# Optimization experiments

Measured on AMD Instinct MI355X. Metric: run time of the kernel, lower is better.

Reference implementation:

```python
import jax, jax.numpy as jnp
import numpy as np

B = 4          # batch
C_FEAT = 32    # shared feature channels
N_PARTS = 24   # body parts
H = 256        # triplane resolution (W = 3*H, three planes concatenated on width)
N_PTS = 8192   # sampled points per batch element
C = C_FEAT + N_PARTS


def setup_inputs() -> dict:
    key = jax.random.key(0)
    k1, k2 = jax.random.split(key)
    triplane = jax.random.normal(k1, (B, C, H, 3 * H), dtype=jnp.float32)
    # canonical coords in [-1, 1], one row per (point, part)
    triplane_coord_3d = jax.random.uniform(
        k2, (B * N_PTS * N_PARTS, 3), dtype=jnp.float32, minval=-1.0, maxval=1.0)
    index = jnp.arange(B * N_PTS, dtype=jnp.int32).reshape(B, N_PTS)
    return {"triplane": triplane, "triplane_coord_3d": triplane_coord_3d, "index": index}


def _bilinear(planes, uv):
    """planes: (B, 3, C, H, H); uv: (B, P, 3, 2) in [-1,1] (x->width, y->height).
    align_corners=False, border-clamped bilinear sample. Returns (B, P, 3, C)."""
    Hs = planes.shape[-1]
    px = (uv[..., 0] + 1.0) * (Hs * 0.5) - 0.5
    py = (uv[..., 1] + 1.0) * (Hs * 0.5) - 0.5
    x0f = jnp.floor(px)
    y0f = jnp.floor(py)
    wx = px - x0f
    wy = py - y0f
    x0 = jnp.clip(x0f.astype(jnp.int32), 0, Hs - 1)
    x1 = jnp.clip(x0f.astype(jnp.int32) + 1, 0, Hs - 1)
    y0 = jnp.clip(y0f.astype(jnp.int32), 0, Hs - 1)
    y1 = jnp.clip(y0f.astype(jnp.int32) + 1, 0, Hs - 1)
    bi = jnp.arange(planes.shape[0])[:, None, None]   # (B,1,1)
    ki = jnp.arange(3)[None, None, :]                 # (1,1,3)

    def g(yi, xi):
        return planes[bi, ki, :, yi, xi]              # (B, P, 3, C)

    return (g(y0, x0) * ((1 - wx) * (1 - wy))[..., None]
            + g(y0, x1) * (wx * (1 - wy))[..., None]
            + g(y1, x0) * ((1 - wx) * wy)[..., None]
            + g(y1, x1) * (wx * wy)[..., None])


def reference(triplane, triplane_coord_3d, index):
    Bq, n = index.shape
    # split width into the 3 concatenated planes -> (B, 3, C, H, H)
    planes = triplane.reshape(Bq, C, H, 3, H).transpose(0, 3, 1, 2, 4)
    # per-(point, part) coordinate rows
    rows = index[..., None] * N_PARTS + jnp.arange(N_PARTS, dtype=index.dtype)  # (B,n,P)
    xyz = triplane_coord_3d[rows]                                 # (B, n, P, 3)
    # plane uv: xy, xz, yz
    uv = jnp.stack([xyz[..., jnp.array([0, 1])],
                    xyz[..., jnp.array([0, 2])],
                    xyz[..., jnp.array([1, 2])]], axis=-2)        # (B, n, P, 3, 2)
    uv = uv.reshape(Bq, n * N_PARTS, 3, 2)
    samp = _bilinear(planes, uv).sum(axis=2)                      # sum over 3 planes -> (B, nP, C)
    samp = samp.reshape(Bq, n, N_PARTS, C)
    part_feature = samp[..., :C_FEAT].mean(axis=-1)               # (B, n, P)
    # part p's probability logit is channel 32+p sampled at part p's coords
    logits = samp[:, :, jnp.arange(N_PARTS), C_FEAT + jnp.arange(N_PARTS)]
    part_prob = jax.nn.softmax(logits, axis=-1)                   # (B, n, P)
    return (part_prob * part_feature).sum(axis=-1)                # (B, n)
```

## Files before the change

### kernel.cpp

```cpp
#include <hip/hip_runtime.h>

#define HS 256
#define W3 768
#define CCH 56
#define CF 32
#define NP 24
#define NPTS 8192
#define PLANE_SZ (HS * W3)

__global__ void tp_mean_kernel(const float* __restrict__ tri,
                               float* __restrict__ M) {
    int i4 = blockIdx.x * blockDim.x + threadIdx.x;
    int b = i4 / (PLANE_SZ / 4);
    int rem = i4 % (PLANE_SZ / 4);
    const float4* in = (const float4*)tri + (size_t)b * CCH * (PLANE_SZ / 4) + rem;
    float4 acc = {0.f, 0.f, 0.f, 0.f};
#pragma unroll
    for (int c = 0; c < CF; ++c) {
        float4 v = in[(size_t)c * (PLANE_SZ / 4)];
        acc.x += v.x; acc.y += v.y; acc.z += v.z; acc.w += v.w;
    }
    const float s = 1.0f / (float)CF;
    acc.x *= s; acc.y *= s; acc.z *= s; acc.w *= s;
    ((float4*)M)[(size_t)b * (PLANE_SZ / 4) + rem] = acc;
}

__global__ __launch_bounds__(192) void tp_sample_kernel(
    const float* __restrict__ tri, const float* __restrict__ coords,
    const int* __restrict__ index, const float* __restrict__ M,
    float* __restrict__ out) {
    __shared__ float s_feat[8][NP];
    __shared__ float s_log[8][NP];

    const int tid = threadIdx.x;
    const int lp = tid / NP;
    const int part = tid % NP;
    const int point = blockIdx.x * 8 + lp;
    const int b = point >> 13;

    const int idx = index[point];
    const int row = idx * NP + part;
    const float x = coords[row * 3 + 0];
    const float y = coords[row * 3 + 1];
    const float z = coords[row * 3 + 2];

    const float us[3] = {x, x, y};
    const float vs[3] = {y, z, z};

    const float* __restrict__ Mb = M + (size_t)b * PLANE_SZ;
    const float* __restrict__ Tb = tri + (size_t)(b * CCH + CF + part) * PLANE_SZ;

    float feat = 0.f, lg = 0.f;
#pragma unroll
    for (int k = 0; k < 3; ++k) {
        const float px = (us[k] + 1.0f) * (HS * 0.5f) - 0.5f;
        const float py = (vs[k] + 1.0f) * (HS * 0.5f) - 0.5f;
        const float x0f = floorf(px);
        const float y0f = floorf(py);
        const float wx = px - x0f;
        const float wy = py - y0f;
        const int x0 = min(max((int)x0f, 0), HS - 1);
        const int x1 = min(max((int)x0f + 1, 0), HS - 1);
        const int y0 = min(max((int)y0f, 0), HS - 1);
        const int y1 = min(max((int)y0f + 1, 0), HS - 1);
        const float w00 = (1.f - wx) * (1.f - wy);
        const float w01 = wx * (1.f - wy);
        const float w10 = (1.f - wx) * wy;
        const float w11 = wx * wy;
        const int o00 = y0 * W3 + k * HS + x0;
        const int o01 = y0 * W3 + k * HS + x1;
        const int o10 = y1 * W3 + k * HS + x0;
        const int o11 = y1 * W3 + k * HS + x1;
        feat += Mb[o00] * w00 + Mb[o01] * w01 + Mb[o10] * w10 + Mb[o11] * w11;
        lg   += Tb[o00] * w00 + Tb[o01] * w01 + Tb[o10] * w10 + Tb[o11] * w11;
    }

    s_feat[lp][part] = feat;
    s_log[lp][part] = lg;
    __syncthreads();

    if (tid < 8) {
        float mx = -1e30f;
#pragma unroll
        for (int j = 0; j < NP; ++j) mx = fmaxf(mx, s_log[tid][j]);
        float se = 0.f, acc = 0.f;
#pragma unroll
        for (int j = 0; j < NP; ++j) {
            const float e = __expf(s_log[tid][j] - mx);
            se += e;
            acc += e * s_feat[tid][j];
        }
        out[blockIdx.x * 8 + tid] = acc / se;
    }
}

extern "C" void kernel_launch(void* const* d_in, const int* in_sizes, int n_in,
                              void* d_out, int out_size, void* d_ws, size_t ws_size,
                              hipStream_t stream) {
    const float* tri = (const float*)d_in[0];
    const float* coords = (const float*)d_in[1];
    const int* index = (const int*)d_in[2];
    float* out = (float*)d_out;
    float* M = (float*)d_ws;

    tp_mean_kernel<<<(4 * PLANE_SZ / 4) / 256, 256, 0, stream>>>(tri, M);

    tp_sample_kernel<<<4096, 192, 0, stream>>>(tri, coords, index, M, out);
}
```

Before: 308.9 us.

## Regroup sampling by (batch, part) slab with XCD-aware block swizzle, separate softmax kernel

The gather kernel now gives each workgroup a single (batch, part) slab of 256 points. All threads then read the same logit channel plane, which should improve L2 locality on the 768 KB part planes. Block indices are swizzled in groups of 8, apparently so that neighbouring logical chunks of a slab land on the same XCD. Per-part features and logits are written to workspace, and a second kernel does the softmax reduction over parts with strided loads. This adds a kernel launch and about 6 MB of extra workspace traffic.

```diff
diff --git a/kernel.cpp b/kernel.cpp
--- a/kernel.cpp
+++ b/kernel.cpp
@@ -7,6 +7,10 @@
 #define NP 24
 #define NPTS 8192
 #define PLANE_SZ (HS * W3)
+#define NB 4
+#define NSLAB (NB * NP)
+#define CHUNKS (NPTS / 256)
+#define NWG_B1 (NSLAB * CHUNKS)
 
 __global__ void tp_mean_kernel(const float* __restrict__ tri,
                                float* __restrict__ M) {
@@ -25,18 +29,18 @@
     ((float4*)M)[(size_t)b * (PLANE_SZ / 4) + rem] = acc;
 }
 
-__global__ __launch_bounds__(192) void tp_sample_kernel(
+__global__ __launch_bounds__(256) void tp_gather_kernel(
     const float* __restrict__ tri, const float* __restrict__ coords,
     const int* __restrict__ index, const float* __restrict__ M,
-    float* __restrict__ out) {
-    __shared__ float s_feat[8][NP];
-    __shared__ float s_log[8][NP];
-
-    const int tid = threadIdx.x;
-    const int lp = tid / NP;
-    const int part = tid % NP;
-    const int point = blockIdx.x * 8 + lp;
-    const int b = point >> 13;
+    float* __restrict__ Wf, float* __restrict__ Wl) {
+    const int phys = blockIdx.x;
+    const int l = (phys & 7) * (NWG_B1 / 8) + (phys >> 3);
+    const int slab = l >> 5;
+    const int chunk = l & 31;
+    const int b = slab / NP;
+    const int part = slab - b * NP;
+    const int n = chunk * 256 + threadIdx.x;
+    const int point = b * NPTS + n;
 
     const int idx = index[point];
     const int row = idx * NP + part;
@@ -75,23 +79,34 @@
         lg   += Tb[o00] * w00 + Tb[o01] * w01 + Tb[o10] * w10 + Tb[o11] * w11;
     }
 
-    s_feat[lp][part] = feat;
-    s_log[lp][part] = lg;
-    __syncthreads();
+    Wf[slab * NPTS + n] = feat;
+    Wl[slab * NPTS + n] = lg;
+}
 
-    if (tid < 8) {
-        float mx = -1e30f;
+__global__ __launch_bounds__(256) void tp_softmax_kernel(
+    const float* __restrict__ Wf, const float* __restrict__ Wl,
+    float* __restrict__ out) {
+    const int g = blockIdx.x * 256 + threadIdx.x;
+    const int b = g >> 13;
+    const int n = g & (NPTS - 1);
+    const float* __restrict__ fb = Wf + (size_t)b * NP * NPTS + n;
+    const float* __restrict__ lb = Wl + (size_t)b * NP * NPTS + n;
+
+    float lv[NP];
+    float mx = -1e30f;
 #pragma unroll
-        for (int j = 0; j < NP; ++j) mx = fmaxf(mx, s_log[tid][j]);
-        float se = 0.f, acc = 0.f;
+    for (int j = 0; j < NP; ++j) {
+        lv[j] = lb[(size_t)j * NPTS];
+        mx = fmaxf(mx, lv[j]);
+    }
+    float se = 0.f, acc = 0.f;
 #pragma unroll
-        for (int j = 0; j < NP; ++j) {
-            const float e = __expf(s_log[tid][j] - mx);
-            se += e;
-            acc += e * s_feat[tid][j];
-        }
-        out[blockIdx.x * 8 + tid] = acc / se;
+    for (int j = 0; j < NP; ++j) {
+        const float e = __expf(lv[j] - mx);
+        se += e;
+        acc += e * fb[(size_t)j * NPTS];
     }
+    out[g] = acc / se;
 }
 
 extern "C" void kernel_launch(void* const* d_in, const int* in_sizes, int n_in,
@@ -101,9 +116,14 @@
     const float* coords = (const float*)d_in[1];
     const int* index = (const int*)d_in[2];
     float* out = (float*)d_out;
-    float* M = (float*)d_ws;
 
-    tp_mean_kernel<<<(4 * PLANE_SZ / 4) / 256, 256, 0, stream>>>(tri, M);
+    float* M  = (float*)d_ws;
+    float* Wf = M + (size_t)NB * PLANE_SZ;
+    float* Wl = Wf + (size_t)NSLAB * NPTS;
 
-    tp_sample_kernel<<<4096, 192, 0, stream>>>(tri, coords, index, M, out);
+    tp_mean_kernel<<<(NB * PLANE_SZ / 4) / 256, 256, 0, stream>>>(tri, M);
+
+    tp_gather_kernel<<<NWG_B1, 256, 0, stream>>>(tri, coords, index, M, Wf, Wl);
+
+    tp_softmax_kernel<<<NPTS * NB / 256, 256, 0, stream>>>(Wf, Wl, out);
 }
```

Result: no change. 303.3 us (-1.8%).

## Split logit sampling into slab-ordered pass fused with mean reduction kernel

Applied to the files above, without the earlier changes.

Moves the per-part logit channel sampling out of the final kernel into a first kernel that also computes the channel mean. Blocks are grouped by (batch, part) slab, and block IDs are swizzled so each block touches only one part plane, which should improve cache locality versus the old per-point gathers across 24 planes. Bilinear taps are fetched as paired 2-float loads with lerp, with two lanes each handling one row and combined by a shuffle. Logits go through a workspace buffer, which adds extra traffic and a dependency on workspace size.

```diff
diff --git a/kernel.cpp b/kernel.cpp
--- a/kernel.cpp
+++ b/kernel.cpp
@@ -7,27 +7,82 @@
 #define NP 24
 #define NPTS 8192
 #define PLANE_SZ (HS * W3)
+#define NB 4
+#define NSLAB (NB * NP)
+#define PTS_PER_BLK 128
+#define CHUNKS (NPTS / PTS_PER_BLK)
+#define NWG_TG (NSLAB * CHUNKS)
+#define NWG_MEAN 768
 
-__global__ void tp_mean_kernel(const float* __restrict__ tri,
-                               float* __restrict__ M) {
-    int i4 = blockIdx.x * blockDim.x + threadIdx.x;
-    int b = i4 / (PLANE_SZ / 4);
-    int rem = i4 % (PLANE_SZ / 4);
-    const float4* in = (const float4*)tri + (size_t)b * CCH * (PLANE_SZ / 4) + rem;
-    float4 acc = {0.f, 0.f, 0.f, 0.f};
+typedef float f2_u __attribute__((ext_vector_type(2), aligned(4)));
+
+__global__ __launch_bounds__(256) void tp_fused1_kernel(
+    const float* __restrict__ tri, const float* __restrict__ coords,
+    const int* __restrict__ index, float* __restrict__ M,
+    float* __restrict__ Wl) {
+    if (blockIdx.x < NWG_MEAN) {
+        int i4 = blockIdx.x * 256 + threadIdx.x;
+        int b = i4 / (PLANE_SZ / 4);
+        int rem = i4 % (PLANE_SZ / 4);
+        const float4* in = (const float4*)tri + (size_t)b * CCH * (PLANE_SZ / 4) + rem;
+        float4 acc = {0.f, 0.f, 0.f, 0.f};
 #pragma unroll
-    for (int c = 0; c < CF; ++c) {
-        float4 v = in[(size_t)c * (PLANE_SZ / 4)];
-        acc.x += v.x; acc.y += v.y; acc.z += v.z; acc.w += v.w;
+        for (int c = 0; c < CF; ++c) {
+            float4 v = in[(size_t)c * (PLANE_SZ / 4)];
+            acc.x += v.x; acc.y += v.y; acc.z += v.z; acc.w += v.w;
+        }
+        const float s = 1.0f / (float)CF;
+        acc.x *= s; acc.y *= s; acc.z *= s; acc.w *= s;
+        ((float4*)M)[(size_t)b * (PLANE_SZ / 4) + rem] = acc;
+        return;
     }
-    const float s = 1.0f / (float)CF;
-    acc.x *= s; acc.y *= s; acc.z *= s; acc.w *= s;
-    ((float4*)M)[(size_t)b * (PLANE_SZ / 4) + rem] = acc;
+    const int phys = blockIdx.x - NWG_MEAN;
+    const int l = (phys & 7) * (NWG_TG / 8) + (phys >> 3);
+    const int slab = l >> 6;
+    const int chunk = l & (CHUNKS - 1);
+    const int b = slab / NP;
+    const int part = slab - b * NP;
+
+    const int lp = threadIdx.x >> 1;
+    const int cy = threadIdx.x & 1;
+
+    const int n = chunk * PTS_PER_BLK + lp;
+    const int point = b * NPTS + n;
+
+    const int idx = index[point];
+    const int row = idx * NP + part;
+    const float x = coords[row * 3 + 0];
+    const float y = coords[row * 3 + 1];
+    const float z = coords[row * 3 + 2];
+
+    const float us[3] = {x, x, y};
+    const float vs[3] = {y, z, z};
+
+    const float* __restrict__ Tb = tri + (size_t)(b * CCH + CF + part) * PLANE_SZ;
+
+    float lg = 0.f;
+#pragma unroll
+    for (int k = 0; k < 3; ++k) {
+        const float px = (us[k] + 1.0f) * (HS * 0.5f) - 0.5f;
+        const float py = (vs[k] + 1.0f) * (HS * 0.5f) - 0.5f;
+        const float x0f = floorf(px);
+        const float y0f = floorf(py);
+        const int bx = min(max((int)x0f, 0), HS - 2);
+        const float wx = fminf(fmaxf(px - (float)bx, 0.f), 1.f);
+        const float wy = py - y0f;
+        const int yc = min(max((int)y0f + cy, 0), HS - 1);
+        const float wyl = cy ? wy : 1.f - wy;
+        const int o = yc * W3 + k * HS + bx;
+        const f2_u tv = *(const f2_u*)(Tb + o);
+        lg += (tv.x + (tv.y - tv.x) * wx) * wyl;
+    }
+    lg += __shfl_xor(lg, 1);
+    if (cy == 0) Wl[slab * NPTS + n] = lg;
 }
 
-__global__ __launch_bounds__(192) void tp_sample_kernel(
-    const float* __restrict__ tri, const float* __restrict__ coords,
-    const int* __restrict__ index, const float* __restrict__ M,
+__global__ __launch_bounds__(192) void tp_fused2_kernel(
+    const float* __restrict__ coords, const int* __restrict__ index,
+    const float* __restrict__ M, const float* __restrict__ Wl,
     float* __restrict__ out) {
     __shared__ float s_feat[8][NP];
     __shared__ float s_log[8][NP];
@@ -37,6 +92,7 @@
     const int part = tid % NP;
     const int point = blockIdx.x * 8 + lp;
     const int b = point >> 13;
+    const int n = point & (NPTS - 1);
 
     const int idx = index[point];
     const int row = idx * NP + part;
@@ -48,35 +104,29 @@
     const float vs[3] = {y, z, z};
 
     const float* __restrict__ Mb = M + (size_t)b * PLANE_SZ;
-    const float* __restrict__ Tb = tri + (size_t)(b * CCH + CF + part) * PLANE_SZ;
 
-    float feat = 0.f, lg = 0.f;
+    float feat = 0.f;
 #pragma unroll
     for (int k = 0; k < 3; ++k) {
         const float px = (us[k] + 1.0f) * (HS * 0.5f) - 0.5f;
         const float py = (vs[k] + 1.0f) * (HS * 0.5f) - 0.5f;
         const float x0f = floorf(px);
         const float y0f = floorf(py);
-        const float wx = px - x0f;
+        const int bx = min(max((int)x0f, 0), HS - 2);
+        const float wx = fminf(fmaxf(px - (float)bx, 0.f), 1.f);
         const float wy = py - y0f;
-        const int x0 = min(max((int)x0f, 0), HS - 1);
-        const int x1 = min(max((int)x0f + 1, 0), HS - 1);
         const int y0 = min(max((int)y0f, 0), HS - 1);
         const int y1 = min(max((int)y0f + 1, 0), HS - 1);
-        const float w00 = (1.f - wx) * (1.f - wy);
-        const float w01 = wx * (1.f - wy);
-        const float w10 = (1.f - wx) * wy;
-        const float w11 = wx * wy;
-        const int o00 = y0 * W3 + k * HS + x0;
-        const int o01 = y0 * W3 + k * HS + x1;
-        const int o10 = y1 * W3 + k * HS + x0;
-        const int o11 = y1 * W3 + k * HS + x1;
-        feat += Mb[o00] * w00 + Mb[o01] * w01 + Mb[o10] * w10 + Mb[o11] * w11;
-        lg   += Tb[o00] * w00 + Tb[o01] * w01 + Tb[o10] * w10 + Tb[o11] * w11;
+        const int o0 = y0 * W3 + k * HS + bx;
+        const int o1 = y1 * W3 + k * HS + bx;
+        const f2_u m0 = *(const f2_u*)(Mb + o0);
+        const f2_u m1 = *(const f2_u*)(Mb + o1);
+        feat += (m0.x + (m0.y - m0.x) * wx) * (1.f - wy)
+              + (m1.x + (m1.y - m1.x) * wx) * wy;
     }
 
     s_feat[lp][part] = feat;
-    s_log[lp][part] = lg;
+    s_log[lp][part] = Wl[(size_t)(b * NP + part) * NPTS + n];
     __syncthreads();
 
     if (tid < 8) {
@@ -101,9 +151,11 @@
     const float* coords = (const float*)d_in[1];
     const int* index = (const int*)d_in[2];
     float* out = (float*)d_out;
-    float* M = (float*)d_ws;
 
-    tp_mean_kernel<<<(4 * PLANE_SZ / 4) / 256, 256, 0, stream>>>(tri, M);
+    float* M  = (float*)d_ws;
+    float* Wl = M + (size_t)NB * PLANE_SZ;
 
-    tp_sample_kernel<<<4096, 192, 0, stream>>>(tri, coords, index, M, out);
+    tp_fused1_kernel<<<NWG_MEAN + NWG_TG, 256, 0, stream>>>(tri, coords, index, M, Wl);
+
+    tp_fused2_kernel<<<NPTS * NB / 8, 192, 0, stream>>>(coords, index, M, Wl, out);
 }
```

Result: faster. 291.7 us (-5.6%).
